# Kernel optimization log

Measured on AMD Instinct MI355X. Metric: run time of the kernel, lower is better.

Reference implementation:

```python
import jax, jax.numpy as jnp
import numpy as np

DIM = 512
HEADS = 16
WS = 8          # window size
SHIFT = 4       # shift size
POSMLP = 32
MLP_HID = 4 * DIM
B = 32
HH = 56
WW = 56
EPS = 1e-5


def setup_inputs() -> dict:
    key = jax.random.key(0)
    ks = jax.random.split(key, 20)
    s = 0.02
    inp = {
        'x': jax.random.normal(ks[0], (B, HH * WW, DIM), jnp.float32),
        'g1': jnp.ones((DIM,), jnp.float32),
        'be1': jnp.zeros((DIM,), jnp.float32),
        'w_qkv': s * jax.random.normal(ks[1], (3 * DIM, DIM), jnp.float32),
        'b_qkv': jnp.zeros((3 * DIM,), jnp.float32),
        'pm_w1': s * jax.random.normal(ks[2], (POSMLP, 2), jnp.float32),
        'pm_b1': jnp.zeros((POSMLP,), jnp.float32),
        'pm_w2': s * jax.random.normal(ks[3], (HEADS, POSMLP), jnp.float32),
        'pm_b2': jnp.zeros((HEADS,), jnp.float32),
        'w_proj': s * jax.random.normal(ks[4], (DIM, DIM), jnp.float32),
        'b_proj': jnp.zeros((DIM,), jnp.float32),
        'g2': jnp.ones((DIM,), jnp.float32),
        'be2': jnp.zeros((DIM,), jnp.float32),
        'w_fc1': s * jax.random.normal(ks[5], (MLP_HID, DIM), jnp.float32),
        'b_fc1': jnp.zeros((MLP_HID,), jnp.float32),
        'w_fc2': s * jax.random.normal(ks[6], (DIM, MLP_HID), jnp.float32),
        'b_fc2': jnp.zeros((DIM,), jnp.float32),
        'H': HH,
        'W': WW,
    }
    return inp


def _layernorm(x, g, b):
    m = jnp.mean(x, -1, keepdims=True)
    v = jnp.mean(jnp.square(x - m), -1, keepdims=True)
    return (x - m) * jax.lax.rsqrt(v + EPS) * g + b


def _shift_mask(H, W, ws, sh):
    # static numpy construction of the (nW, N, N) 0/-100 shift mask
    img = np.zeros((H, W), np.float32)
    cnt = 0
    for hs in (slice(0, -ws), slice(-ws, -sh), slice(-sh, None)):
        for wsl in (slice(0, -ws), slice(-ws, -sh), slice(-sh, None)):
            img[hs, wsl] = cnt
            cnt += 1
    mw = img.reshape(H // ws, ws, W // ws, ws).transpose(0, 2, 1, 3).reshape(-1, ws * ws)
    diff = mw[:, None, :] - mw[:, :, None]
    return jnp.asarray(np.where(diff != 0, -100.0, 0.0).astype(np.float32))


def _pos_bias(ws, pm_w1, pm_b1, pm_w2, pm_b2):
    # log-CPB relative position bias computed by a tiny MLP -> (heads, N, N)
    g = jnp.stack(jnp.meshgrid(jnp.arange(ws), jnp.arange(ws), indexing='ij'))
    coords = g.reshape(2, -1).astype(jnp.float32)        # [2, N]
    d = coords[:, :, None] - coords[:, None, :]          # [2, N, N]
    d = jnp.sign(d) * jnp.log1p(jnp.abs(d))
    h = jax.nn.relu(jnp.einsum('cnm,oc->onm', d, pm_w1) + pm_b1[:, None, None])
    return jnp.einsum('onm,ho->hnm', h, pm_w2) + pm_b2[:, None, None]


def reference(x, g1, be1, w_qkv, b_qkv, pm_w1, pm_b1, pm_w2, pm_b2,
              w_proj, b_proj, g2, be2, w_fc1, b_fc1, w_fc2, b_fc2, H, W):
    ws, sh, nh = WS, SHIFT, HEADS
    Bb, L, C = x.shape
    hd = C // nh
    scale = hd ** -0.5
    N = ws * ws
    nWh, nWw = H // ws, W // ws
    nW = nWh * nWw

    shortcut = x
    xn = _layernorm(x, g1, be1).reshape(Bb, H, W, C)
    xn = jnp.roll(xn, (-sh, -sh), axis=(1, 2))
    # window partition -> (B*nW, N, C)
    xw = xn.reshape(Bb, nWh, ws, nWw, ws, C).transpose(0, 1, 3, 2, 4, 5).reshape(-1, N, C)

    qkv = (xw @ w_qkv.T + b_qkv).reshape(-1, N, 3, nh, hd).transpose(2, 0, 3, 1, 4)
    q, k, v = qkv[0], qkv[1], qkv[2]           # each (B*nW, nh, N, hd)

    attn = jnp.einsum('bhnd,bhmd->bhnm', q * scale, k)
    attn = attn + _pos_bias(ws, pm_w1, pm_b1, pm_w2, pm_b2)[None]

    mask = _shift_mask(H, W, ws, sh)           # (nW, N, N)
    attn = attn.reshape(Bb, nW, nh, N, N) + mask[None, :, None]
    attn = jax.nn.softmax(attn.reshape(-1, nh, N, N), axis=-1)

    out = jnp.einsum('bhnm,bhmd->bhnd', attn, v).transpose(0, 2, 1, 3).reshape(-1, N, C)
    out = out @ w_proj.T + b_proj

    # window reverse + roll back
    out = out.reshape(Bb, nWh, nWw, ws, ws, C).transpose(0, 1, 3, 2, 4, 5).reshape(Bb, H, W, C)
    out = jnp.roll(out, (sh, sh), axis=(1, 2)).reshape(Bb, L, C)

    x1 = shortcut + out
    h = jax.nn.gelu(_layernorm(x1, g2, be2) @ w_fc1.T + b_fc1, approximate=False)
    return x1 + (h @ w_fc2.T + b_fc2)
```

## Files before the change

### kernel.cpp

```cpp
#include <hip/hip_runtime.h>
#include <math.h>

typedef __bf16 bf16;
typedef bf16 bf16x4 __attribute__((ext_vector_type(4)));
typedef bf16 bf16x8 __attribute__((ext_vector_type(8)));
typedef float f32x4 __attribute__((ext_vector_type(4)));

#define MFMA_BF16(a, b, c) __builtin_amdgcn_mfma_f32_16x16x32_bf16((a), (b), (c), 0, 0, 0)
#define GLDS16(gp, lp)                                                            \
  __builtin_amdgcn_global_load_lds((__attribute__((address_space(1))) void*)(gp), \
                                   (__attribute__((address_space(3))) void*)(lp), 16, 0, 0)
#define VMCNT(N) asm volatile("s_waitcnt vmcnt(" #N ")" ::: "memory")
#define LGKM(N) asm volatile("s_waitcnt lgkmcnt(" #N ")" ::: "memory")
#define SBAR __builtin_amdgcn_s_barrier()
#define SCHED0 __builtin_amdgcn_sched_barrier(0)

static constexpr int kDim   = 512;
static constexpr int kHeads = 16;
static constexpr int kHd    = 32;
static constexpr int kNt    = 64;
static constexpr int kNw    = 49;
static constexpr int kL     = 3136;
static constexpr int kToks  = 100352;
static constexpr int kWins  = 1568;
static constexpr int kHid   = 2048;
static constexpr size_t kQS = (size_t)kWins * kHeads * kNt * kHd;

__global__ __launch_bounds__(256) void wconv_kernel(const float* __restrict__ s,
                                                    bf16* __restrict__ d, int n8) {
  int i = blockIdx.x * 256 + threadIdx.x;
  if (i >= n8) return;
  const float4 a = *(const float4*)(s + i * 8);
  const float4 b = *(const float4*)(s + i * 8 + 4);
  bf16x8 o;
  o[0] = (bf16)a.x; o[1] = (bf16)a.y; o[2] = (bf16)a.z; o[3] = (bf16)a.w;
  o[4] = (bf16)b.x; o[5] = (bf16)b.y; o[6] = (bf16)b.z; o[7] = (bf16)b.w;
  *(bf16x8*)(d + i * 8) = o;
}

__global__ void posbias_kernel(const float* __restrict__ w1, const float* __restrict__ b1,
                               const float* __restrict__ w2, const float* __restrict__ b2,
                               float* __restrict__ tbl) {
  int idx = blockIdx.x * 256 + threadIdx.x;
  if (idx >= kHeads * kNt * kNt) return;
  int h = idx >> 12, n = (idx >> 6) & 63, m = idx & 63;
  float dr = (float)((n >> 3) - (m >> 3));
  float dc = (float)((n & 7) - (m & 7));
  dr = (dr > 0.f ? 1.f : (dr < 0.f ? -1.f : 0.f)) * log1pf(fabsf(dr));
  dc = (dc > 0.f ? 1.f : (dc < 0.f ? -1.f : 0.f)) * log1pf(fabsf(dc));
  float acc = b2[h];
  for (int o = 0; o < 32; ++o) {
    float hv = w1[o * 2] * dr + w1[o * 2 + 1] * dc + b1[o];
    acc += w2[h * 32 + o] * fmaxf(hv, 0.f);
  }
  tbl[idx] = acc;
}

template <int MODE>
__global__ __launch_bounds__(256) void ln_kernel(const float* __restrict__ x,
                                                 const float* __restrict__ g,
                                                 const float* __restrict__ be,
                                                 bf16* __restrict__ o) {
  const int t = blockIdx.x * 4 + (threadIdx.x >> 6);
  const int lane = threadIdx.x & 63;
  size_t src;
  if (MODE == 0) {
    const int win = t >> 6, n = t & 63;
    const int b = win / kNw, wi = win % kNw;
    const int h0 = ((wi / 7) * 8 + (n >> 3) + 4) % 56;
    const int w0 = ((wi % 7) * 8 + (n & 7) + 4) % 56;
    src = ((size_t)b * kL + h0 * 56 + w0) * kDim;
  } else {
    src = (size_t)t * kDim;
  }
  const float4 a = *(const float4*)(x + src + lane * 8);
  const float4 bq = *(const float4*)(x + src + lane * 8 + 4);
  float xf[8] = {a.x, a.y, a.z, a.w, bq.x, bq.y, bq.z, bq.w};
  float s = 0.f, s2 = 0.f;
#pragma unroll
  for (int j = 0; j < 8; ++j) { s += xf[j]; s2 += xf[j] * xf[j]; }
#pragma unroll
  for (int off = 32; off > 0; off >>= 1) { s += __shfl_xor(s, off); s2 += __shfl_xor(s2, off); }
  const float mean = s * (1.f / 512.f);
  const float rstd = rsqrtf(s2 * (1.f / 512.f) - mean * mean + 1e-5f);
  const float4 ga = *(const float4*)(g + lane * 8);
  const float4 gb = *(const float4*)(g + lane * 8 + 4);
  const float4 ba = *(const float4*)(be + lane * 8);
  const float4 bb = *(const float4*)(be + lane * 8 + 4);
  const float gv[8] = {ga.x, ga.y, ga.z, ga.w, gb.x, gb.y, gb.z, gb.w};
  const float bv[8] = {ba.x, ba.y, ba.z, ba.w, bb.x, bb.y, bb.z, bb.w};
  bf16x8 ov;
#pragma unroll
  for (int j = 0; j < 8; ++j) ov[j] = (bf16)((xf[j] - mean) * rstd * gv[j] + bv[j]);
  *(bf16x8*)(o + (size_t)t * kDim + lane * 8) = ov;
}

#define LOAD_A(dst, CB, KH, MB)                                        \
  _Pragma("unroll") for (int i = 0; i < 4; ++i)                        \
      dst[i] = *(const bf16x8*)(&L[CB][0][KH][aoff + (MB + i) * 512]);
#define LOAD_B(dst, CB, KH)                                            \
  _Pragma("unroll") for (int i = 0; i < 4; ++i)                        \
      dst[i] = *(const bf16x8*)(&L[CB][1][KH][boff + i * 512]);
#define MFMAS(MB, AF, BF)                                              \
  SCHED0;                                                              \
  __builtin_amdgcn_s_setprio(1);                                       \
  _Pragma("unroll") for (int mi = 0; mi < 4; ++mi)                     \
  _Pragma("unroll") for (int ni = 0; ni < 4; ++ni)                     \
      acc[MB + mi][ni] = MFMA_BF16(BF[ni], AF[mi], acc[MB + mi][ni]);  \
  __builtin_amdgcn_s_setprio(0)

template <int EPI>
__global__ __launch_bounds__(512, 2) void gemm256(const bf16* __restrict__ A, const bf16* __restrict__ B,
                                                  const float* __restrict__ bias, void* __restrict__ Cv,
                                                  const float* __restrict__ extra, int N, int K) {
  __shared__ __align__(16) bf16 L[2][2][2][8192];
  const int nbn = N >> 8;
  const int nwg = (int)gridDim.x;
  int wg = (int)blockIdx.x;
  {
    const int q = nwg >> 3, r = nwg & 7;
    const int xcd = wg & 7, loc = wg >> 3;
    wg = (xcd < r ? xcd * (q + 1) : r * (q + 1) + (xcd - r) * q) + loc;
  }
  const int bm = wg / nbn, bn = wg % nbn;
  const int tid = (int)threadIdx.x;
  const int wave = tid >> 6, lane = tid & 63;
  const int wm2 = wave >> 2, wn4 = wave & 3;
  const int quad = lane >> 4, l16 = lane & 15;

  const int sl0 = tid, sl1 = 512 + tid;
  const int rp0 = sl0 >> 3, ls0 = (sl0 & 7) ^ (rp0 & 7);
  const int rp1 = sl1 >> 3, ls1 = (sl1 & 7) ^ (rp1 & 7);
  const int row0 = rp0 * 2 + (ls0 >> 2), c0 = ls0 & 3;
  const int row1 = rp1 * 2 + (ls1 >> 2), c1 = ls1 & 3;
  const bf16* pa0 = A + (size_t)(bm * 256 + row0) * K + c0 * 8;
  const bf16* pa1 = A + (size_t)(bm * 256 + row1) * K + c1 * 8;
  const bf16* pb0 = B + (size_t)(bn * 256 + row0) * K + c0 * 8;
  const bf16* pb1 = B + (size_t)(bn * 256 + row1) * K + c1 * 8;

  const int ar = wm2 * 128 + l16, arp = ar >> 1;
  const int aoff = (arp * 8 + ((((ar & 1) << 2) | quad) ^ (arp & 7))) * 8;
  const int br = wn4 * 64 + l16, brp = br >> 1;
  const int boff = (brp * 8 + ((((br & 1) << 2) | quad) ^ (brp & 7))) * 8;

  f32x4 acc[8][4] = {};
  bf16x8 af0[4], af1[4], bfr0[4], bfr1[4];

  GLDS16(pa0, &L[0][0][0][sl0 * 8]);
  GLDS16(pa1, &L[0][0][0][sl1 * 8]);
  GLDS16(pb0, &L[0][1][0][sl0 * 8]);
  GLDS16(pb1, &L[0][1][0][sl1 * 8]);
  GLDS16(pa0 + 32, &L[0][0][1][sl0 * 8]);
  GLDS16(pa1 + 32, &L[0][0][1][sl1 * 8]);
  GLDS16(pb0 + 32, &L[0][1][1][sl0 * 8]);
  GLDS16(pb1 + 32, &L[0][1][1][sl1 * 8]);
  VMCNT(4);
  SBAR;
  LOAD_A(af0, 0, 0, 0);
  LOAD_B(bfr0, 0, 0);

#pragma unroll 2
  for (int kt = 0; kt < K - 64; kt += 64) {
    const int cb = (kt >> 6) & 1, nb = cb ^ 1;
    const int kn = kt + 64;
    LOAD_A(af1, cb, 0, 4);
    GLDS16(pa0 + kn, &L[nb][0][0][sl0 * 8]);
    GLDS16(pa1 + kn, &L[nb][0][0][sl1 * 8]);
    LGKM(4);
    MFMAS(0, af0, bfr0);
    VMCNT(2);
    SBAR;
    LOAD_A(af0, cb, 1, 0);
    LOAD_B(bfr1, cb, 1);
    GLDS16(pb0 + kn, &L[nb][1][0][sl0 * 8]);
    GLDS16(pb1 + kn, &L[nb][1][0][sl1 * 8]);
    LGKM(8);
    MFMAS(4, af1, bfr0);
    SBAR;
    LOAD_A(af1, cb, 1, 4);
    GLDS16(pa0 + kn + 32, &L[nb][0][1][sl0 * 8]);
    GLDS16(pa1 + kn + 32, &L[nb][0][1][sl1 * 8]);
    LGKM(4);
    MFMAS(0, af0, bfr1);
    VMCNT(2);
    SBAR;
    LOAD_A(af0, nb, 0, 0);
    LOAD_B(bfr0, nb, 0);
    GLDS16(pb0 + kn + 32, &L[nb][1][1][sl0 * 8]);
    GLDS16(pb1 + kn + 32, &L[nb][1][1][sl1 * 8]);
    LGKM(8);
    MFMAS(4, af1, bfr1);
    SBAR;
  }
  {
    const int cb = ((K >> 6) - 1) & 1;
    LOAD_A(af1, cb, 0, 4);
    LGKM(4);
    MFMAS(0, af0, bfr0);
    VMCNT(0);
    SBAR;
    LOAD_A(af0, cb, 1, 0);
    LOAD_B(bfr1, cb, 1);
    LGKM(8);
    MFMAS(4, af1, bfr0);
    SBAR;
    LOAD_A(af1, cb, 1, 4);
    LGKM(4);
    MFMAS(0, af0, bfr1);
    SBAR;
    LGKM(0);
    MFMAS(4, af1, bfr1);
  }

  bf16* Cb = (bf16*)Cv;
  float* Cf = (float*)Cv;
#pragma unroll
  for (int mi = 0; mi < 8; ++mi) {
    const int row = bm * 256 + wm2 * 128 + mi * 16 + l16;
#pragma unroll
    for (int ni = 0; ni < 4; ++ni) {
      const int colb = bn * 256 + wn4 * 64 + ni * 16 + quad * 4;
      const float4 bq = *(const float4*)(bias + colb);
      const float bbv[4] = {bq.x, bq.y, bq.z, bq.w};
      float v4[4];
#pragma unroll
      for (int r = 0; r < 4; ++r) v4[r] = acc[mi][ni][r] + bbv[r];
      if constexpr (EPI == 1) {
        const int which = colb >> 9, head = (colb >> 5) & 15, d = colb & 31;
        const int win = row >> 6, n = row & 63;
        bf16x4 ov;
#pragma unroll
        for (int r = 0; r < 4; ++r) ov[r] = (bf16)v4[r];
        *(bf16x4*)(Cb + (size_t)which * kQS + (((size_t)win * kHeads + head) * kNt + n) * kHd + d) = ov;
      } else if constexpr (EPI == 2) {
        bf16x4 ov;
#pragma unroll
        for (int r = 0; r < 4; ++r) {
          const float g = 0.5f * v4[r] * (1.f + erff(v4[r] * 0.70710678118654752f));
          ov[r] = (bf16)g;
        }
        *(bf16x4*)(Cb + (size_t)row * N + colb) = ov;
      } else if constexpr (EPI == 3) {
        const float4 ex = *(const float4*)(extra + (size_t)row * N + colb);
        float4 o4 = {v4[0] + ex.x, v4[1] + ex.y, v4[2] + ex.z, v4[3] + ex.w};
        *(float4*)(Cf + (size_t)row * N + colb) = o4;
      } else {
        const int win = row >> 6, n = row & 63;
        const int b = win / kNw, wi = win % kNw;
        const int h0 = ((wi / 7) * 8 + (n >> 3) + 4) % 56;
        const int w0 = ((wi % 7) * 8 + (n & 7) + 4) % 56;
        const size_t dst = ((size_t)b * kL + h0 * 56 + w0) * kDim + colb;
        const float4 ex = *(const float4*)(extra + dst);
        float4 o4 = {v4[0] + ex.x, v4[1] + ex.y, v4[2] + ex.z, v4[3] + ex.w};
        *(float4*)(Cf + dst) = o4;
      }
    }
  }
}

__device__ __forceinline__ int reg3(int x) { return x < 48 ? 0 : (x < 52 ? 1 : 2); }

__global__ __launch_bounds__(128) void attn_kernel(const bf16* __restrict__ qkv,
                                                   const float* __restrict__ ptbl,
                                                   bf16* __restrict__ out) {
  __shared__ float Sb[2][64 * 65];
  __shared__ float Rs[2][64];
  __shared__ bf16  Pb[2][64 * 72];
  __shared__ bf16  Vt[2][32 * 72];
  const int w = threadIdx.x >> 6, lane = threadIdx.x & 63;
  const int gwh = blockIdx.x * 2 + w;
  const int win = gwh >> 4, h = gwh & 15;
  const int quad = lane >> 4, l16 = lane & 15;
  const bf16* q = qkv + ((size_t)win * kHeads + h) * (kNt * kHd);
  const bf16* k = q + kQS;
  const bf16* v = q + 2 * kQS;

#pragma unroll
  for (int i = 0; i < 4; ++i) {
    const int row = i * 16 + (lane >> 2);
    const int d0 = (lane & 3) * 8;
    bf16x8 vv = *(const bf16x8*)(v + row * kHd + d0);
#pragma unroll
    for (int j = 0; j < 8; ++j) Vt[w][(d0 + j) * 72 + row] = vv[j];
  }

  bf16x8 qf[4], kf[4];
#pragma unroll
  for (int i = 0; i < 4; ++i) qf[i] = *(const bf16x8*)(q + (i * 16 + l16) * kHd + quad * 8);
#pragma unroll
  for (int j = 0; j < 4; ++j) kf[j] = *(const bf16x8*)(k + (j * 16 + l16) * kHd + quad * 8);
  f32x4 sa[4][4] = {};
#pragma unroll
  for (int i = 0; i < 4; ++i)
#pragma unroll
    for (int j = 0; j < 4; ++j) sa[i][j] = MFMA_BF16(qf[i], kf[j], sa[i][j]);

  const int wi = win % kNw;
  const int hb = (wi / 7) * 8, wb = (wi % 7) * 8;
  const float* bh = ptbl + h * 4096;
#pragma unroll
  for (int i = 0; i < 4; ++i) {
#pragma unroll
    for (int j = 0; j < 4; ++j) {
      const int ct = j * 16 + l16;
      const int crg = reg3(hb + (ct >> 3)) * 3 + reg3(wb + (ct & 7));
#pragma unroll
      for (int r = 0; r < 4; ++r) {
        const int rt = i * 16 + quad * 4 + r;
        const int rrg = reg3(hb + (rt >> 3)) * 3 + reg3(wb + (rt & 7));
        float sv = sa[i][j][r] * 0.17677669529663687f + bh[rt * 64 + ct];
        if (rrg != crg) sv -= 100.f;
        Sb[w][rt * 65 + ct] = sv;
      }
    }
  }
  __syncthreads();

  float mx = -1e30f;
  for (int i = 0; i < 64; ++i) mx = fmaxf(mx, Sb[w][lane * 65 + i]);
  float sum = 0.f;
  for (int i = 0; i < 64; ++i) {
    const float p = __expf(Sb[w][lane * 65 + i] - mx);
    sum += p;
    Pb[w][lane * 72 + i] = (bf16)p;
  }
  Rs[w][lane] = 1.f / sum;
  __syncthreads();

  f32x4 oa[4][2] = {};
#pragma unroll
  for (int kk = 0; kk < 2; ++kk) {
    bf16x8 pf[4], vf[2];
#pragma unroll
    for (int mi = 0; mi < 4; ++mi)
      pf[mi] = *(const bf16x8*)(&Pb[w][(mi * 16 + l16) * 72 + kk * 32 + quad * 8]);
#pragma unroll
    for (int nj = 0; nj < 2; ++nj)
      vf[nj] = *(const bf16x8*)(&Vt[w][(nj * 16 + l16) * 72 + kk * 32 + quad * 8]);
#pragma unroll
    for (int mi = 0; mi < 4; ++mi)
#pragma unroll
      for (int nj = 0; nj < 2; ++nj) oa[mi][nj] = MFMA_BF16(pf[mi], vf[nj], oa[mi][nj]);
  }
#pragma unroll
  for (int mi = 0; mi < 4; ++mi)
#pragma unroll
    for (int nj = 0; nj < 2; ++nj)
#pragma unroll
      for (int r = 0; r < 4; ++r) {
        const int row = mi * 16 + quad * 4 + r;
        const int col = nj * 16 + l16;
        out[((size_t)win * kNt + row) * kDim + h * kHd + col] = (bf16)(oa[mi][nj][r] * Rs[w][row]);
      }
}

extern "C" void kernel_launch(void* const* d_in, const int* in_sizes, int n_in,
                              void* d_out, int out_size, void* d_ws, size_t ws_size,
                              hipStream_t stream) {
  (void)in_sizes; (void)n_in; (void)out_size; (void)ws_size;
  const float* x      = (const float*)d_in[0];
  const float* g1     = (const float*)d_in[1];
  const float* be1    = (const float*)d_in[2];
  const float* w_qkv  = (const float*)d_in[3];
  const float* b_qkv  = (const float*)d_in[4];
  const float* pm_w1  = (const float*)d_in[5];
  const float* pm_b1  = (const float*)d_in[6];
  const float* pm_w2  = (const float*)d_in[7];
  const float* pm_b2  = (const float*)d_in[8];
  const float* w_proj = (const float*)d_in[9];
  const float* b_proj = (const float*)d_in[10];
  const float* g2     = (const float*)d_in[11];
  const float* be2    = (const float*)d_in[12];
  const float* w_fc1  = (const float*)d_in[13];
  const float* b_fc1  = (const float*)d_in[14];
  const float* w_fc2  = (const float*)d_in[15];
  const float* b_fc2  = (const float*)d_in[16];
  float* out = (float*)d_out;
  char* ws = (char*)d_ws;

  constexpr size_t OFF_WB   = 1u << 20;
  constexpr size_t OFF_XW   = OFF_WB + (8u << 20);
  constexpr size_t SZ_ACT   = (size_t)kToks * kDim * 2;
  constexpr size_t OFF_QKV  = OFF_XW + SZ_ACT;
  float* biastbl = (float*)ws;
  bf16* wqb = (bf16*)(ws + OFF_WB);
  bf16* wpb = wqb + 786432;
  bf16* w1b = wpb + 262144;
  bf16* w2b = w1b + 1048576;
  bf16* xw    = (bf16*)(ws + OFF_XW);
  bf16* attnb = xw;
  bf16* xn2   = xw;
  bf16* qkvb = (bf16*)(ws + OFF_QKV);
  float* x1  = (float*)(ws + OFF_QKV);
  bf16* hbuf = (bf16*)(ws + OFF_QKV + (size_t)kToks * kDim * 4);

  wconv_kernel<<<dim3(786432 / 2048), dim3(256), 0, stream>>>(w_qkv, wqb, 786432 / 8);
  wconv_kernel<<<dim3(262144 / 2048), dim3(256), 0, stream>>>(w_proj, wpb, 262144 / 8);
  wconv_kernel<<<dim3(1048576 / 2048), dim3(256), 0, stream>>>(w_fc1, w1b, 1048576 / 8);
  wconv_kernel<<<dim3(1048576 / 2048), dim3(256), 0, stream>>>(w_fc2, w2b, 1048576 / 8);
  posbias_kernel<<<dim3(256), dim3(256), 0, stream>>>(pm_w1, pm_b1, pm_w2, pm_b2, biastbl);
  ln_kernel<0><<<dim3(kToks / 4), dim3(256), 0, stream>>>(x, g1, be1, xw);
  gemm256<1><<<dim3((kToks / 256) * (1536 / 256)), dim3(512), 0, stream>>>(
      xw, wqb, b_qkv, qkvb, nullptr, 1536, 512);
  attn_kernel<<<dim3(kWins * kHeads / 2), dim3(128), 0, stream>>>(qkvb, biastbl, attnb);
  gemm256<4><<<dim3((kToks / 256) * (512 / 256)), dim3(512), 0, stream>>>(
      attnb, wpb, b_proj, x1, x, 512, 512);
  ln_kernel<1><<<dim3(kToks / 4), dim3(256), 0, stream>>>(x1, g2, be2, xn2);
  constexpr int kChunk = kToks / 4;
  for (int c = 0; c < 4; ++c) {
    const size_t ro = (size_t)c * kChunk * kDim;
    gemm256<2><<<dim3((kChunk / 256) * (kHid / 256)), dim3(512), 0, stream>>>(
        xn2 + ro, w1b, b_fc1, hbuf, nullptr, kHid, 512);
    gemm256<3><<<dim3((kChunk / 256) * (512 / 256)), dim3(512), 0, stream>>>(
        hbuf, w2b, b_fc2, out + ro, x1 + ro, 512, kHid);
  }
}
```

Baseline: 1.674 ms.

## Restructure GEMM main loop to one barrier per k-tile and relax launch bounds

The GEMM k-loop now issues all global-to-LDS prefetches for the next tile up front, then runs the four MFMA phases reading only from the current LDS buffer, with one vmcnt wait and barrier per iteration instead of four. Launch bounds are relaxed from 2 to 1 workgroups per CU, which gives the compiler more registers. The aim is to cut barrier stalls and fine-grained sync inside the loop. The cost is less overlap between the next tile's loads and compute at the tile boundary, and possibly lower occupancy.

```diff
diff --git a/kernel.cpp b/kernel.cpp
--- a/kernel.cpp
+++ b/kernel.cpp
@@ -110,7 +110,7 @@
   __builtin_amdgcn_s_setprio(0)
 
 template <int EPI>
-__global__ __launch_bounds__(512, 2) void gemm256(const bf16* __restrict__ A, const bf16* __restrict__ B,
+__global__ __launch_bounds__(512, 1) void gemm256(const bf16* __restrict__ A, const bf16* __restrict__ B,
                                                   const float* __restrict__ bias, void* __restrict__ Cv,
                                                   const float* __restrict__ extra, int N, int K) {
   __shared__ __align__(16) bf16 L[2][2][2][8192];
@@ -144,7 +144,7 @@
   const int boff = (brp * 8 + ((((br & 1) << 2) | quad) ^ (brp & 7))) * 8;
 
   f32x4 acc[8][4] = {};
-  bf16x8 af0[4], af1[4], bfr0[4], bfr1[4];
+  bf16x8 afA[4], afB[4], bfr0[4], bfr1[4];
 
   GLDS16(pa0, &L[0][0][0][sl0 * 8]);
   GLDS16(pa1, &L[0][0][0][sl1 * 8]);
@@ -154,62 +154,54 @@
   GLDS16(pa1 + 32, &L[0][0][1][sl1 * 8]);
   GLDS16(pb0 + 32, &L[0][1][1][sl0 * 8]);
   GLDS16(pb1 + 32, &L[0][1][1][sl1 * 8]);
-  VMCNT(4);
+  VMCNT(0);
   SBAR;
-  LOAD_A(af0, 0, 0, 0);
-  LOAD_B(bfr0, 0, 0);
 
 #pragma unroll 2
   for (int kt = 0; kt < K - 64; kt += 64) {
     const int cb = (kt >> 6) & 1, nb = cb ^ 1;
     const int kn = kt + 64;
-    LOAD_A(af1, cb, 0, 4);
+    LOAD_A(afA, cb, 0, 0);
+    LOAD_B(bfr0, cb, 0);
     GLDS16(pa0 + kn, &L[nb][0][0][sl0 * 8]);
     GLDS16(pa1 + kn, &L[nb][0][0][sl1 * 8]);
-    LGKM(4);
-    MFMAS(0, af0, bfr0);
-    VMCNT(2);
-    SBAR;
-    LOAD_A(af0, cb, 1, 0);
-    LOAD_B(bfr1, cb, 1);
     GLDS16(pb0 + kn, &L[nb][1][0][sl0 * 8]);
     GLDS16(pb1 + kn, &L[nb][1][0][sl1 * 8]);
-    LGKM(8);
-    MFMAS(4, af1, bfr0);
-    SBAR;
-    LOAD_A(af1, cb, 1, 4);
     GLDS16(pa0 + kn + 32, &L[nb][0][1][sl0 * 8]);
     GLDS16(pa1 + kn + 32, &L[nb][0][1][sl1 * 8]);
-    LGKM(4);
-    MFMAS(0, af0, bfr1);
-    VMCNT(2);
-    SBAR;
-    LOAD_A(af0, nb, 0, 0);
-    LOAD_B(bfr0, nb, 0);
     GLDS16(pb0 + kn + 32, &L[nb][1][1][sl0 * 8]);
     GLDS16(pb1 + kn + 32, &L[nb][1][1][sl1 * 8]);
+    LOAD_A(afB, cb, 0, 4);
+    LGKM(4);
+    MFMAS(0, afA, bfr0);
+    LOAD_A(afA, cb, 1, 0);
+    LOAD_B(bfr1, cb, 1);
     LGKM(8);
-    MFMAS(4, af1, bfr1);
+    MFMAS(4, afB, bfr0);
+    LOAD_A(afB, cb, 1, 4);
+    LGKM(4);
+    MFMAS(0, afA, bfr1);
+    LGKM(0);
+    MFMAS(4, afB, bfr1);
+    VMCNT(0);
     SBAR;
   }
   {
     const int cb = ((K >> 6) - 1) & 1;
-    LOAD_A(af1, cb, 0, 4);
+    LOAD_A(afA, cb, 0, 0);
+    LOAD_B(bfr0, cb, 0);
+    LOAD_A(afB, cb, 0, 4);
     LGKM(4);
-    MFMAS(0, af0, bfr0);
-    VMCNT(0);
-    SBAR;
-    LOAD_A(af0, cb, 1, 0);
+    MFMAS(0, afA, bfr0);
+    LOAD_A(afA, cb, 1, 0);
     LOAD_B(bfr1, cb, 1);
     LGKM(8);
-    MFMAS(4, af1, bfr0);
-    SBAR;
-    LOAD_A(af1, cb, 1, 4);
+    MFMAS(4, afB, bfr0);
+    LOAD_A(afB, cb, 1, 4);
     LGKM(4);
-    MFMAS(0, af0, bfr1);
-    SBAR;
+    MFMAS(0, afA, bfr1);
     LGKM(0);
-    MFMAS(4, af1, bfr1);
+    MFMAS(4, afB, bfr1);
   }
 
   bf16* Cb = (bf16*)Cv;
```

New measurement: 1.669 ms. No clear change (-0.3%).
